# Performance work log

Hardware: AMD Instinct MI355X
Metric: run time of the kernel (lower is better)

## Reference

```python
import jax, jax.numpy as jnp
import numpy as np

B, N, C = 2, 2048, 768
H = 12
HD = C // H  # 64


def setup_inputs() -> dict:
    key = jax.random.key(0)
    ks = jax.random.split(key, 6)
    s = 0.02
    x = jax.random.normal(ks[0], (B, N, C), dtype=jnp.float32)
    xpos = jnp.arange(B * N, dtype=jnp.int64).reshape(B, N) % N
    W_qkv = jax.random.normal(ks[1], (3 * C, C), dtype=jnp.float32) * s
    b_qkv = jnp.zeros((3 * C,), dtype=jnp.float32)
    W_proj = jax.random.normal(ks[2], (C, C), dtype=jnp.float32) * s
    b_proj = jnp.zeros((C,), dtype=jnp.float32)
    return {"x": x, "xpos": xpos, "W_qkv": W_qkv, "b_qkv": b_qkv,
            "W_proj": W_proj, "b_proj": b_proj}


def reference(x, xpos, W_qkv, b_qkv, W_proj, b_proj):
    # rope is None in this configuration -> xpos is unused, matching torch module.
    Bx, Nx, Cx = x.shape
    scale = (Cx // H) ** -0.5
    qkv = x @ W_qkv.T + b_qkv                     # [B, N, 3C]
    qkv = qkv.reshape(Bx, Nx, 3, H, HD)
    q = jnp.einsum('bnhd->bhnd', qkv[:, :, 0])    # [B, H, N, HD]
    k = jnp.einsum('bnhd->bhnd', qkv[:, :, 1])
    v = jnp.einsum('bnhd->bhnd', qkv[:, :, 2])
    attn = jnp.einsum('bhnd,bhmd->bhnm', q, k) * scale  # [B, H, N, N]
    attn = jax.nn.softmax(attn, axis=-1)
    out = jnp.einsum('bhnm,bhmd->bhnd', attn, v)  # [B, H, N, HD]
    out = jnp.einsum('bhnd->bnhd', out).reshape(Bx, Nx, Cx)
    return out @ W_proj.T + b_proj
```

## Files before the change

kernel.cpp:

```cpp
#include <hip/hip_runtime.h>
#include <hip/hip_bf16.h>


typedef _Float16 half8 __attribute__((ext_vector_type(8)));
typedef _Float16 half4_t __attribute__((ext_vector_type(4)));
typedef float floatx4 __attribute__((ext_vector_type(4)));
typedef float floatx16 __attribute__((ext_vector_type(16)));
typedef unsigned int uintx4 __attribute__((ext_vector_type(4)));
typedef unsigned int uintx2 __attribute__((ext_vector_type(2)));

#define SCALE_LOG2E 0.1803368801111204f

constexpr int XH_OFF    = 0;
constexpr int WQKV_OFF  = XH_OFF + 4096 * 768;
constexpr int WPROJ_OFF = WQKV_OFF + 2304 * 768;
constexpr int QK_OFF    = WPROJ_OFF + 768 * 768;
constexpr int VTH_OFF   = QK_OFF + 4096 * 1536;
constexpr int PO_OFF    = VTH_OFF + 24 * 64 * 2048;
constexpr int PSTAT_OFF = PO_OFF + 2 * 24 * 2048 * 64;

__device__ __forceinline__ void gl16(const _Float16* g, _Float16* l) {
  __builtin_amdgcn_global_load_lds(
      (const __attribute__((address_space(1))) unsigned int*)g,
      (__attribute__((address_space(3))) unsigned int*)l, 16, 0, 0);
}

__global__ __launch_bounds__(256) void cvt_all(const float* __restrict__ x,
                                               const float* __restrict__ wqkv,
                                               const float* __restrict__ wproj,
                                               _Float16* __restrict__ ws) {
  constexpr int n1 = 4096 * 768 / 4;
  constexpr int n2 = 2304 * 768 / 4;
  int i = blockIdx.x * 256 + threadIdx.x;
  const float* src; _Float16* dst; int j;
  if (i < n1)           { src = x;     dst = ws + XH_OFF;    j = i; }
  else if (i < n1 + n2) { src = wqkv;  dst = ws + WQKV_OFF;  j = i - n1; }
  else                  { src = wproj; dst = ws + WPROJ_OFF; j = i - n1 - n2; }
  floatx4 f = *(const floatx4*)(src + 4 * j);
  half4_t h;
  h[0] = (_Float16)f[0]; h[1] = (_Float16)f[1];
  h[2] = (_Float16)f[2]; h[3] = (_Float16)f[3];
  *(half4_t*)(dst + 4 * j) = h;
}

__global__ __launch_bounds__(256) void qkv_gemm(const _Float16* __restrict__ xh,
                                                const _Float16* __restrict__ wh,
                                                const float* __restrict__ bias,
                                                _Float16* __restrict__ qkh,
                                                _Float16* __restrict__ vth) {
  __shared__ __align__(16) _Float16 sA[128 * 64];
  __shared__ __align__(16) _Float16 sB[128 * 64];
  const int tid = threadIdx.x;
  const int nblk = blockIdx.x % 18, mblk = blockIdx.x / 18;
  const int lane = tid & 63, w = tid >> 6;
  const int lane15 = lane & 15, quad = lane >> 4;
  const int lrow = lane >> 3, lchunk = lane & 7;
  const int wq = w >> 1, wn = w & 1;

  floatx4 acc[4][4];
#pragma unroll
  for (int mt = 0; mt < 4; ++mt)
#pragma unroll
    for (int nt = 0; nt < 4; ++nt) acc[mt][nt] = (floatx4){0.f, 0.f, 0.f, 0.f};

  for (int kt = 0; kt < 12; ++kt) {
    if (kt) __syncthreads();
#pragma unroll
    for (int i = 0; i < 8; ++i) {
      int g = i * 32 + w * 8;
      if (g < 128)
        gl16(xh + (mblk * 128 + g + lrow) * 768 + kt * 64 + lchunk * 8, sA + g * 64);
      else
        gl16(wh + (nblk * 128 + (g - 128) + lrow) * 768 + kt * 64 + lchunk * 8,
             sB + (g - 128) * 64);
    }
    __syncthreads();
#pragma unroll
    for (int ks = 0; ks < 2; ++ks) {
      half8 af[4], bf[4];
#pragma unroll
      for (int mt = 0; mt < 4; ++mt)
        af[mt] = *(const half8*)(sA + (wq * 64 + mt * 16 + lane15) * 64 + ks * 32 + quad * 8);
#pragma unroll
      for (int nt = 0; nt < 4; ++nt)
        bf[nt] = *(const half8*)(sB + (wn * 64 + nt * 16 + lane15) * 64 + ks * 32 + quad * 8);
#pragma unroll
      for (int mt = 0; mt < 4; ++mt)
#pragma unroll
        for (int nt = 0; nt < 4; ++nt)
          acc[mt][nt] = __builtin_amdgcn_mfma_f32_16x16x32_f16(af[mt], bf[nt], acc[mt][nt], 0, 0, 0);
    }
  }

  const int mbase = mblk * 128 + wq * 64;
#pragma unroll
  for (int nt = 0; nt < 4; ++nt) {
    int cbase = nblk * 128 + wn * 64 + nt * 16;
    float bv = bias[cbase + lane15];
    if (cbase < 1536) {
      int col = cbase + lane15;
      float sc = (cbase < 768) ? SCALE_LOG2E : 1.0f;
#pragma unroll
      for (int mt = 0; mt < 4; ++mt)
#pragma unroll
        for (int r = 0; r < 4; ++r) {
          int token = mbase + mt * 16 + quad * 4 + r;
          qkh[token * 1536 + col] = (_Float16)((acc[mt][nt][r] + bv) * sc);
        }
    } else {
      int dcol = cbase - 1536 + lane15;
      int h = dcol >> 6, d = dcol & 63;
#pragma unroll
      for (int mt = 0; mt < 4; ++mt) {
        int tok0 = mbase + mt * 16 + quad * 4;
        int b = tok0 >> 11, n0 = tok0 & 2047;
        int bh = b * 12 + h;
        half4_t hv;
#pragma unroll
        for (int r = 0; r < 4; ++r) hv[r] = (_Float16)(acc[mt][nt][r] + bv);
        *(half4_t*)(vth + (bh * 64 + d) * 2048 + n0) = hv;
      }
    }
  }
}

__global__ __launch_bounds__(256, 3) void attn_fused(const _Float16* __restrict__ qkh,
                                                     const _Float16* __restrict__ vth,
                                                     _Float16* __restrict__ pO,
                                                     float* __restrict__ pL) {
  __shared__ __align__(16) _Float16 sK[2][64 * 64];
  __shared__ __align__(16) _Float16 sVT[2][64 * 64];
  const int tid = threadIdx.x;
  const int bx = blockIdx.x;
  const int bh = bx % 24;
  const int rest = bx / 24;
  const int ks = rest & 1, qt = rest >> 1;
  const int b = bh / 12, h = bh % 12;
  const int lane = tid & 63, w = tid >> 6;
  const int q = lane & 31, hi = lane >> 5;

  const int qkbase = b * 2048 * 1536 + h * 64;
  const int qrow = qt * 128 + w * 32 + q;

  half8 qf[4];
#pragma unroll
  for (int c = 0; c < 4; ++c)
    qf[c] = *(const half8*)(qkh + qkbase + qrow * 1536 + c * 16 + hi * 8);

  const int srow = tid >> 2, sc = tid & 3;
  const int key0 = ks * 1024;
  const _Float16* kp = qkh + qkbase + 768 + (key0 + srow) * 1536 + sc * 8;
  const _Float16* vp = vth + (bh * 64 + srow) * 2048 + key0 + sc * 8;
  const int sw0 = srow * 64 + ((sc ^ (srow & 7)) * 8);
  const int sw1 = srow * 64 + (((sc + 4) ^ (srow & 7)) * 8);

  floatx16 O[2];
#pragma unroll
  for (int dg = 0; dg < 2; ++dg)
#pragma unroll
    for (int i = 0; i < 16; ++i) O[dg][i] = 0.f;
  float lrow = 0.f;

  half8 rk0 = *(const half8*)kp, rk1 = *(const half8*)(kp + 32);
  half8 rv0 = *(const half8*)vp, rv1 = *(const half8*)(vp + 32);
  kp += 64 * 1536; vp += 64;
  { _Float16* nK = &sK[0][0]; _Float16* nV = &sVT[0][0];
    *(half8*)(nK + sw0) = rk0; *(half8*)(nK + sw1) = rk1;
    *(half8*)(nV + sw0) = rv0; *(half8*)(nV + sw1) = rv1; }
  rk0 = *(const half8*)kp; rk1 = *(const half8*)(kp + 32);
  rv0 = *(const half8*)vp; rv1 = *(const half8*)(vp + 32);
  kp += 64 * 1536; vp += 64;

  for (int kt = 0; kt < 16; ++kt) {
    __syncthreads();
    const _Float16* cK = &sK[kt & 1][0];
    const _Float16* cV = &sVT[kt & 1][0];
    if (kt < 15) {
      _Float16* nK = &sK[(kt + 1) & 1][0];
      _Float16* nV = &sVT[(kt + 1) & 1][0];
      *(half8*)(nK + sw0) = rk0; *(half8*)(nK + sw1) = rk1;
      *(half8*)(nV + sw0) = rv0; *(half8*)(nV + sw1) = rv1;
      if (kt < 14) {
        rk0 = *(const half8*)kp; rk1 = *(const half8*)(kp + 32);
        rv0 = *(const half8*)vp; rv1 = *(const half8*)(vp + 32);
        kp += 64 * 1536; vp += 64;
      }
    }

    float rsum = 0.f;
#pragma unroll
    for (int og = 0; og < 2; ++og) {
      floatx16 s;
#pragma unroll
      for (int i = 0; i < 16; ++i) s[i] = 0.f;
      const int krow = og * 32 + q;
#pragma unroll
      for (int c = 0; c < 4; ++c) {
        half8 kf = *(const half8*)(cK + krow * 64 + (((c * 2 + hi) ^ (krow & 7)) * 8));
        s = __builtin_amdgcn_mfma_f32_32x32x16_f16(kf, qf[c], s, 0, 0, 0);
      }

#pragma unroll
      for (int mm = 0; mm < 2; ++mm) {
        const int rb = mm * 8;
        float e0 = __builtin_amdgcn_exp2f(s[rb + 0]);
        float e1 = __builtin_amdgcn_exp2f(s[rb + 1]);
        float e2 = __builtin_amdgcn_exp2f(s[rb + 2]);
        float e3 = __builtin_amdgcn_exp2f(s[rb + 3]);
        float e4 = __builtin_amdgcn_exp2f(s[rb + 4]);
        float e5 = __builtin_amdgcn_exp2f(s[rb + 5]);
        float e6 = __builtin_amdgcn_exp2f(s[rb + 6]);
        float e7 = __builtin_amdgcn_exp2f(s[rb + 7]);
        rsum += ((e0 + e1) + (e2 + e3)) + ((e4 + e5) + (e6 + e7));
        unsigned ua = __builtin_bit_cast(unsigned, __builtin_amdgcn_cvt_pkrtz(e0, e1));
        unsigned ub = __builtin_bit_cast(unsigned, __builtin_amdgcn_cvt_pkrtz(e2, e3));
        unsigned uc = __builtin_bit_cast(unsigned, __builtin_amdgcn_cvt_pkrtz(e4, e5));
        unsigned ud = __builtin_bit_cast(unsigned, __builtin_amdgcn_cvt_pkrtz(e6, e7));
        uintx2 sAC = __builtin_amdgcn_permlane32_swap(ua, uc, false, false);
        uintx2 sBD = __builtin_amdgcn_permlane32_swap(ub, ud, false, false);
        uintx4 u; u[0] = sAC[0]; u[1] = sBD[0]; u[2] = sAC[1]; u[3] = sBD[1];
        half8 bfrag = __builtin_bit_cast(half8, u);

        const int rc2 = (og * 2 + mm) * 2 + hi;
#pragma unroll
        for (int dg = 0; dg < 2; ++dg) {
          const int vrow = dg * 32 + q;
          half8 vf = *(const half8*)(cV + vrow * 64 + ((rc2 ^ (vrow & 7)) * 8));
          O[dg] = __builtin_amdgcn_mfma_f32_32x32x16_f16(vf, bfrag, O[dg], 0, 0, 0);
        }
      }
    }
    lrow += rsum;
  }

  const int prow = (ks * 24 + bh) * 2048 + qt * 128 + w * 32;
#pragma unroll
  for (int dg = 0; dg < 2; ++dg)
#pragma unroll
    for (int g2 = 0; g2 < 4; ++g2) {
      half4_t hv;
#pragma unroll
      for (int e = 0; e < 4; ++e) hv[e] = (_Float16)O[dg][g2 * 4 + e];
      *(half4_t*)(pO + (prow + q) * 64 + dg * 32 + g2 * 8 + hi * 4) = hv;
    }
  lrow += __shfl_xor(lrow, 32, 64);
  if (lane < 32) pL[prow + lane] = lrow;
}

__global__ __launch_bounds__(256) void proj_gemm(const _Float16* __restrict__ pO,
                                                 const float* __restrict__ pL,
                                                 const _Float16* __restrict__ wh,
                                                 const float* __restrict__ bias,
                                                 float* __restrict__ out) {
  __shared__ __align__(16) _Float16 sA[64 * 72];
  __shared__ __align__(16) _Float16 sB[128 * 64];
  const int tid = threadIdx.x;
  const int nblk = blockIdx.x % 6, mblk = blockIdx.x / 6;
  const int lane = tid & 63, w = tid >> 6;
  const int lane15 = lane & 15, quad = lane >> 4;
  const int lrow = lane >> 3, lchunk = lane & 7;
  const int arow = tid >> 2, achk = tid & 3;
  const int tok0 = mblk * 64;
  const int b = tok0 >> 11, tokl = tok0 & 2047;

  floatx4 acc[4][2];
#pragma unroll
  for (int mt = 0; mt < 4; ++mt)
#pragma unroll
    for (int nt = 0; nt < 2; ++nt) acc[mt][nt] = (floatx4){0.f, 0.f, 0.f, 0.f};

  for (int kt = 0; kt < 12; ++kt) {
    const int bh = b * 12 + kt;
    const int row1 = bh * 2048 + tokl + arow;
    const int row2 = (24 + bh) * 2048 + tokl + arow;
    float f = 1.0f / (pL[row1] + pL[row2]);

    if (kt) __syncthreads();
#pragma unroll
    for (int i = 0; i < 4; ++i) {
      int g = w * 32 + 8 * i;
      gl16(wh + (nblk * 128 + g + lrow) * 768 + kt * 64 + lchunk * 8, sB + g * 64);
    }
#pragma unroll
    for (int cc = 0; cc < 2; ++cc) {
      int c8 = achk + 4 * cc;
      half8 o1 = *(const half8*)(pO + row1 * 64 + c8 * 8);
      half8 o2 = *(const half8*)(pO + row2 * 64 + c8 * 8);
      half8 o;
#pragma unroll
      for (int e = 0; e < 8; ++e)
        o[e] = (_Float16)(f * ((float)o1[e] + (float)o2[e]));
      *(half8*)(sA + arow * 72 + c8 * 8) = o;
    }
    __syncthreads();

#pragma unroll
    for (int ksplit = 0; ksplit < 2; ++ksplit) {
      half8 af[4], bf[2];
#pragma unroll
      for (int mt = 0; mt < 4; ++mt)
        af[mt] = *(const half8*)(sA + (mt * 16 + lane15) * 72 + ksplit * 32 + quad * 8);
#pragma unroll
      for (int nt = 0; nt < 2; ++nt)
        bf[nt] = *(const half8*)(sB + (w * 32 + nt * 16 + lane15) * 64 + ksplit * 32 + quad * 8);
#pragma unroll
      for (int mt = 0; mt < 4; ++mt)
#pragma unroll
        for (int nt = 0; nt < 2; ++nt)
          acc[mt][nt] = __builtin_amdgcn_mfma_f32_16x16x32_f16(af[mt], bf[nt], acc[mt][nt], 0, 0, 0);
    }
  }

  const int mbase = mblk * 64;
#pragma unroll
  for (int nt = 0; nt < 2; ++nt) {
    int col = nblk * 128 + w * 32 + nt * 16 + lane15;
    float bv = bias[col];
#pragma unroll
    for (int mt = 0; mt < 4; ++mt)
#pragma unroll
      for (int r = 0; r < 4; ++r) {
        int token = mbase + mt * 16 + quad * 4 + r;
        out[token * 768 + col] = acc[mt][nt][r] + bv;
      }
  }
}

extern "C" void kernel_launch(void* const* d_in, const int* in_sizes, int n_in,
                              void* d_out, int out_size, void* d_ws, size_t ws_size,
                              hipStream_t stream) {
  const float* x     = (const float*)d_in[0];
  const float* wqkv  = (const float*)d_in[2];
  const float* bqkv  = (const float*)d_in[3];
  const float* wproj = (const float*)d_in[4];
  const float* bproj = (const float*)d_in[5];
  float* out = (float*)d_out;

  _Float16* ws = (_Float16*)d_ws;
  _Float16* xh     = ws + XH_OFF;
  _Float16* wqkvh  = ws + WQKV_OFF;
  _Float16* wprojh = ws + WPROJ_OFF;
  _Float16* qkh    = ws + QK_OFF;
  _Float16* vth    = ws + VTH_OFF;
  _Float16* pO     = ws + PO_OFF;
  float*    pL     = (float*)(ws + PSTAT_OFF);

  constexpr int total_v4 = (4096 * 768 + 2304 * 768 + 768 * 768) / 4;
  cvt_all<<<total_v4 / 256, 256, 0, stream>>>(x, wqkv, wproj, ws);
  qkv_gemm<<<32 * 18, 256, 0, stream>>>(xh, wqkvh, bqkv, qkh, vth);
  attn_fused<<<24 * 32, 256, 0, stream>>>(qkh, vth, pO, pL);
  proj_gemm<<<64 * 6, 256, 0, stream>>>(pO, pL, wprojh, bproj, out);
}
```

Before: 161.2 us.

## Stream attention K/V tiles straight to LDS and raise occupancy bound

The attention kernel's K and V^T tiles now go from global memory directly into shared memory with global_load_lds DMA. This replaces the old path of loading into registers and then writing to LDS. The XOR swizzle moves into the global source column index, so the LDS layout the MFMA reads expect stays the same. Dropping the staging registers lets the launch bound rise from 3 to 4 blocks per SIMD group, aiming at more latency hiding. The cost is that the prefetch now relies on the barrier to wait for the asynchronous LDS writes, and the tighter register budget could cause spills.

```diff
diff --git a/kernel.cpp b/kernel.cpp
--- a/kernel.cpp
+++ b/kernel.cpp
@@ -124,7 +124,7 @@
   }
 }
 
-__global__ __launch_bounds__(256, 3) void attn_fused(const _Float16* __restrict__ qkh,
+__global__ __launch_bounds__(256, 4) void attn_fused(const _Float16* __restrict__ qkh,
                                                      const _Float16* __restrict__ vth,
                                                      _Float16* __restrict__ pO,
                                                      float* __restrict__ pL) {
@@ -147,12 +147,11 @@
   for (int c = 0; c < 4; ++c)
     qf[c] = *(const half8*)(qkh + qkbase + qrow * 1536 + c * 16 + hi * 8);
 
-  const int srow = tid >> 2, sc = tid & 3;
+  const int l3 = lane >> 3;
+  const int lc = (lane & 7) ^ l3;
   const int key0 = ks * 1024;
-  const _Float16* kp = qkh + qkbase + 768 + (key0 + srow) * 1536 + sc * 8;
-  const _Float16* vp = vth + (bh * 64 + srow) * 2048 + key0 + sc * 8;
-  const int sw0 = srow * 64 + ((sc ^ (srow & 7)) * 8);
-  const int sw1 = srow * 64 + (((sc + 4) ^ (srow & 7)) * 8);
+  const _Float16* kbase = qkh + qkbase + 768 + (key0 + w * 8 + l3) * 1536 + lc * 8;
+  const _Float16* vbase = vth + (bh * 64 + w * 8 + l3) * 2048 + key0 + lc * 8;
 
   floatx16 O[2];
 #pragma unroll
@@ -161,31 +160,24 @@
     for (int i = 0; i < 16; ++i) O[dg][i] = 0.f;
   float lrow = 0.f;
 
-  half8 rk0 = *(const half8*)kp, rk1 = *(const half8*)(kp + 32);
-  half8 rv0 = *(const half8*)vp, rv1 = *(const half8*)(vp + 32);
-  kp += 64 * 1536; vp += 64;
-  { _Float16* nK = &sK[0][0]; _Float16* nV = &sVT[0][0];
-    *(half8*)(nK + sw0) = rk0; *(half8*)(nK + sw1) = rk1;
-    *(half8*)(nV + sw0) = rv0; *(half8*)(nV + sw1) = rv1; }
-  rk0 = *(const half8*)kp; rk1 = *(const half8*)(kp + 32);
-  rv0 = *(const half8*)vp; rv1 = *(const half8*)(vp + 32);
-  kp += 64 * 1536; vp += 64;
+  auto stage = [&](int kt, int bufsel) {
+    _Float16* dK = (_Float16*)sK[bufsel] + w * 512;
+    _Float16* dV = (_Float16*)sVT[bufsel] + w * 512;
+    const _Float16* kc = kbase + kt * 64 * 1536;
+    const _Float16* vc = vbase + kt * 64;
+    gl16(kc, dK);
+    gl16(kc + 32 * 1536, dK + 2048);
+    gl16(vc, dV);
+    gl16(vc + 32 * 2048, dV + 2048);
+  };
+
+  stage(0, 0);
 
   for (int kt = 0; kt < 16; ++kt) {
     __syncthreads();
+    if (kt < 15) stage(kt + 1, (kt + 1) & 1);
     const _Float16* cK = &sK[kt & 1][0];
     const _Float16* cV = &sVT[kt & 1][0];
-    if (kt < 15) {
-      _Float16* nK = &sK[(kt + 1) & 1][0];
-      _Float16* nV = &sVT[(kt + 1) & 1][0];
-      *(half8*)(nK + sw0) = rk0; *(half8*)(nK + sw1) = rk1;
-      *(half8*)(nV + sw0) = rv0; *(half8*)(nV + sw1) = rv1;
-      if (kt < 14) {
-        rk0 = *(const half8*)kp; rk1 = *(const half8*)(kp + 32);
-        rv0 = *(const half8*)vp; rv1 = *(const half8*)(vp + 32);
-        kp += 64 * 1536; vp += 64;
-      }
-    }
 
     float rsum = 0.f;
 #pragma unroll
```

Result: slower. 165.3 us (+2.6%).
